# Optimization experiments

Measured on AMD Instinct MI355X. Metric: run time of the kernel, lower is better.

## Reference

```python
import jax, jax.numpy as jnp
import numpy as np

LN_EPS = 1e-5

def _layernorm(x, g, b):
    mu = jnp.mean(x, axis=-1, keepdims=True)
    var = jnp.var(x, axis=-1, keepdims=True)
    return (x - mu) * jax.lax.rsqrt(var + LN_EPS) * g + b

def setup_inputs() -> dict:
    key = jax.random.key(0)
    ks = jax.random.split(key, 8)
    B, N, n, m, a = 4096, 50000, 1024, 16384, 256
    return {
        "x": jax.random.normal(ks[0], (B, n), dtype=jnp.float32),
        "X_data": jax.random.normal(ks[1], (N, n), dtype=jnp.float32),
        "memory_indices": jax.random.randint(ks[2], (m,), 0, N, dtype=jnp.int64)
            if jax.config.jax_enable_x64 else jax.random.randint(ks[2], (m,), 0, N, dtype=jnp.int32),
        "W_q": jax.random.normal(ks[3], (a, n), dtype=jnp.float32) / np.sqrt(n),
        "W_k": jax.random.normal(ks[4], (a, n), dtype=jnp.float32) / np.sqrt(n),
        "W_v": jax.random.normal(ks[5], (n, n), dtype=jnp.float32) / np.sqrt(n),
        "g_q": jnp.ones((a,), jnp.float32), "b_q": jnp.zeros((a,), jnp.float32),
        "g_k": jnp.ones((a,), jnp.float32), "b_k": jnp.zeros((a,), jnp.float32),
        "g_v": jnp.ones((n,), jnp.float32), "b_v": jnp.zeros((n,), jnp.float32),
    }

def reference(x, X_data, memory_indices, W_q, W_k, W_v, g_q, b_q, g_k, b_k, g_v, b_v):
    # Gather memory bank rows: [m, n]
    X_cross = X_data[memory_indices]
    n = x.shape[-1]
    # preprocess(): scalar normalizer so mean row norm ~= sqrt(n) (SAE convention)
    C = jnp.mean(jnp.linalg.norm(X_cross, axis=-1)) / jnp.sqrt(jnp.asarray(n, x.dtype))
    X_cross = X_cross / C
    xs = x / C
    # QKV projections (Linear, no bias) + per-stream LayerNorm
    q = _layernorm(xs @ W_q.T, g_q, b_q)        # [B, a]
    k = _layernorm(X_cross @ W_k.T, g_k, b_k)   # [m, a]
    v = _layernorm(X_cross @ W_v.T, g_v, b_v)   # [m, n]
    # scaled dot-product attention over the memory bank
    scale = 1.0 / np.sqrt(q.shape[-1])
    attn = jax.nn.softmax(jnp.einsum('ba,ma->bm', q, k) * scale, axis=-1)  # [B, m]
    x_hat = attn @ v                             # [B, n]
    return (xs, x_hat, attn, v)
```

## Files before the change

### kernel.cpp

```cpp
#include <hip/hip_runtime.h>
#include <math.h>

typedef _Float16 hlf4 __attribute__((ext_vector_type(4)));
typedef _Float16 hlf8 __attribute__((ext_vector_type(8)));
typedef float f32x4 __attribute__((ext_vector_type(4)));

static __device__ __forceinline__ void gl_lds16(const void* g, void* l) {
    __builtin_amdgcn_global_load_lds(
        (const __attribute__((address_space(1))) unsigned int*)g,
        (__attribute__((address_space(3))) unsigned int*)l, 16, 0, 0);
}

static __device__ __forceinline__ float blk_sum(float v) {
    __shared__ float sm[256];
    int tid = threadIdx.x;
    sm[tid] = v; __syncthreads();
#pragma unroll
    for (int s = 128; s > 0; s >>= 1) {
        if (tid < s) sm[tid] += sm[tid + s];
        __syncthreads();
    }
    float r = sm[0]; __syncthreads();
    return r;
}

static __device__ __forceinline__ float blk_max(float v) {
    __shared__ float sm[256];
    int tid = threadIdx.x;
    sm[tid] = v; __syncthreads();
#pragma unroll
    for (int s = 128; s > 0; s >>= 1) {
        if (tid < s) sm[tid] = fmaxf(sm[tid], sm[tid + s]);
        __syncthreads();
    }
    float r = sm[0]; __syncthreads();
    return r;
}

__global__ __launch_bounds__(256) void k_row_norms(
    const float* __restrict__ X, const int* __restrict__ idx,
    float* __restrict__ norms, int n) {
    long long r = idx[blockIdx.x];
    const float* xr = X + r * (long long)n;
    float s = 0.f;
    for (int k = threadIdx.x * 4; k < n; k += 256 * 4) {
        float4 v = *(const float4*)(xr + k);
        s = fmaf(v.x, v.x, s); s = fmaf(v.y, v.y, s);
        s = fmaf(v.z, v.z, s); s = fmaf(v.w, v.w, s);
    }
    float tot = blk_sum(s);
    if (threadIdx.x == 0) norms[blockIdx.x] = sqrtf(tot);
}

__global__ __launch_bounds__(256) void k_cinv(
    const float* __restrict__ norms, int m, int n, float* __restrict__ cinv) {
    float s = 0.f;
    for (int i = threadIdx.x; i < m; i += 256) s += norms[i];
    float tot = blk_sum(s);
    if (threadIdx.x == 0) cinv[0] = (float)m * sqrtf((float)n) / tot;
}

__global__ __launch_bounds__(256) void k_scale2(
    const float* __restrict__ x, const float* __restrict__ cinv,
    float* __restrict__ y, _Float16* __restrict__ yh, long long total4) {
    float c = cinv[0];
    long long i = blockIdx.x * 256ll + threadIdx.x;
    long long stride = (long long)gridDim.x * 256ll;
    for (; i < total4; i += stride) {
        float4 v = ((const float4*)x)[i];
        float4 w = {v.x * c, v.y * c, v.z * c, v.w * c};
        ((float4*)y)[i] = w;
        hlf4 o = {(_Float16)v.x, (_Float16)v.y, (_Float16)v.z, (_Float16)v.w};
        ((hlf4*)yh)[i] = o;
    }
}

__global__ __launch_bounds__(256) void k_gather_cvt(
    const float* __restrict__ X, const int* __restrict__ idx,
    _Float16* __restrict__ out, int n) {
    long long r = idx[blockIdx.x];
    const float* src = X + r * (long long)n;
    _Float16* dst = out + (long long)blockIdx.x * n;
    for (int k = threadIdx.x * 4; k < n; k += 256 * 4) {
        float4 v = *(const float4*)(src + k);
        hlf4 o = {(_Float16)v.x, (_Float16)v.y, (_Float16)v.z, (_Float16)v.w};
        *(hlf4*)(dst + k) = o;
    }
}

__global__ __launch_bounds__(256) void k_cvt(
    const float* __restrict__ in, _Float16* __restrict__ out, long long n4,
    float sc) {
    long long i = blockIdx.x * 256ll + threadIdx.x;
    long long stride = (long long)gridDim.x * 256ll;
    for (; i < n4; i += stride) {
        float4 v = ((const float4*)in)[i];
        hlf4 o = {(_Float16)(v.x * sc), (_Float16)(v.y * sc),
                  (_Float16)(v.z * sc), (_Float16)(v.w * sc)};
        ((hlf4*)out)[i] = o;
    }
}

__global__ __launch_bounds__(256) void k_tcvt(
    const float* __restrict__ in, _Float16* __restrict__ out, int R, int Cc) {
    __shared__ _Float16 t[32][34];
    int tx = threadIdx.x & 31, ty = threadIdx.x >> 5;
    int c0 = blockIdx.x * 32, r0 = blockIdx.y * 32;
#pragma unroll
    for (int i = 0; i < 32; i += 8)
        t[ty + i][tx] = (_Float16)in[(long long)(r0 + ty + i) * Cc + c0 + tx];
    __syncthreads();
#pragma unroll
    for (int i = 0; i < 32; i += 8)
        out[(long long)(c0 + ty + i) * R + r0 + tx] = t[tx][ty + i];
}

template <int MODE>
__global__ __launch_bounds__(256) void k_gemm4(
    const _Float16* __restrict__ A, int lda,
    const _Float16* __restrict__ B, int ldb,
    void* __restrict__ Cc, long long ldc, int K,
    float* __restrict__ part, long long zstride) {
    __shared__ _Float16 Ah[2][4096];
    __shared__ _Float16 Bh[2][4096];
    const int tid = threadIdx.x;
    const long long m0 = (long long)blockIdx.x * 128;
    const long long n0 = (long long)blockIdx.y * 128;
    const int KC = K / gridDim.z;
    const int kbase = blockIdx.z * KC;
    const int lane = tid & 63, wv = tid >> 6;
    const int wm = (wv >> 1) * 64, wn = (wv & 1) * 64;
    const int fr = lane & 15, fq = lane >> 4;

    const int s0 = tid, s1 = tid + 256;
    const int r0s = s0 >> 2, r1s = s1 >> 2;
    const int g0 = (((s0 & 3) ^ (r0s & 3)) << 3);
    const int g1 = (((s1 & 3) ^ (r1s & 3)) << 3);
    const _Float16* A0 = A + (m0 + r0s) * (long long)lda + kbase + g0;
    const _Float16* A1 = A + (m0 + r1s) * (long long)lda + kbase + g1;
    const _Float16* B0 = B + (n0 + r0s) * (long long)ldb + kbase + g0;
    const _Float16* B1 = B + (n0 + r1s) * (long long)ldb + kbase + g1;

    f32x4 acc[4][4] = {};

    const int NT = KC / 32;
    {
        gl_lds16(A0, &Ah[0][wv * 512]);
        gl_lds16(A1, &Ah[0][2048 + wv * 512]);
        gl_lds16(B0, &Bh[0][wv * 512]);
        gl_lds16(B1, &Bh[0][2048 + wv * 512]);
    }
    __syncthreads();

    for (int kt = 0; kt < NT; ++kt) {
        const int cur = kt & 1;
        if (kt + 1 < NT) {
            const int nx = cur ^ 1;
            const long long ko = (long long)(kt + 1) * 32;
            gl_lds16(A0 + ko, &Ah[nx][wv * 512]);
            gl_lds16(A1 + ko, &Ah[nx][2048 + wv * 512]);
            gl_lds16(B0 + ko, &Bh[nx][wv * 512]);
            gl_lds16(B1 + ko, &Bh[nx][2048 + wv * 512]);
        }
        hlf8 af[4], bf[4];
#pragma unroll
        for (int i = 0; i < 4; ++i) {
            const int r = wm + i * 16 + fr;
            af[i] = *(const hlf8*)&Ah[cur][r * 32 + ((fq ^ (r & 3)) << 3)];
        }
#pragma unroll
        for (int j = 0; j < 4; ++j) {
            const int r = wn + j * 16 + fr;
            bf[j] = *(const hlf8*)&Bh[cur][r * 32 + ((fq ^ (r & 3)) << 3)];
        }
#pragma unroll
        for (int i = 0; i < 4; ++i)
#pragma unroll
            for (int j = 0; j < 4; ++j)
                acc[i][j] = __builtin_amdgcn_mfma_f32_16x16x32_f16(af[i], bf[j], acc[i][j], 0, 0, 0);
        __syncthreads();
    }

    if constexpr (MODE == 1) {
        _Float16* op = (_Float16*)Cc;
#pragma unroll
        for (int i = 0; i < 4; ++i)
#pragma unroll
            for (int j = 0; j < 4; ++j) {
                _Float16* cp = op + (m0 + wm + i * 16 + fq * 4) * ldc + (n0 + wn + j * 16 + fr);
#pragma unroll
                for (int r = 0; r < 4; ++r)
                    cp[(long long)r * ldc] = (_Float16)__expf(acc[i][j][r] - 5.0f);
            }
    } else {
        float* outp = (gridDim.z == 1) ? (float*)Cc : (part + (long long)blockIdx.z * zstride);
#pragma unroll
        for (int i = 0; i < 4; ++i)
#pragma unroll
            for (int j = 0; j < 4; ++j) {
                float* cp = outp + (m0 + wm + i * 16 + fq * 4) * ldc + (n0 + wn + j * 16 + fr);
#pragma unroll
                for (int r = 0; r < 4; ++r) cp[(long long)r * ldc] = acc[i][j][r];
            }
    }
}

__global__ __launch_bounds__(256) void k_redux(
    const float* __restrict__ part, float* __restrict__ out,
    long long n4, long long zs4, int Z,
    const float* __restrict__ invs, int rowdiv4) {
    long long i = blockIdx.x * 256ll + threadIdx.x;
    long long stride = (long long)gridDim.x * 256ll;
    for (; i < n4; i += stride) {
        float4 s = ((const float4*)part)[i];
        for (int z = 1; z < Z; ++z) {
            float4 t = ((const float4*)part)[i + z * zs4];
            s.x += t.x; s.y += t.y; s.z += t.z; s.w += t.w;
        }
        if (invs) {
            float iv = invs[i / rowdiv4];
            s.x *= iv; s.y *= iv; s.z *= iv; s.w *= iv;
        }
        ((float4*)out)[i] = s;
    }
}

template <int CNT>
__global__ __launch_bounds__(256) void k_layernorm(
    float* __restrict__ Y, const float* __restrict__ g,
    const float* __restrict__ b, int W) {
    float* yr = Y + (long long)blockIdx.x * W;
    float v[CNT];
    float s = 0.f;
#pragma unroll
    for (int i = 0; i < CNT; ++i) {
        v[i] = yr[threadIdx.x + (i << 8)];
        s += v[i];
    }
    float mu = blk_sum(s) / (float)W;
    float sq = 0.f;
#pragma unroll
    for (int i = 0; i < CNT; ++i) {
        float d = v[i] - mu;
        sq = fmaf(d, d, sq);
    }
    float var = blk_sum(sq) / (float)W;
    float rs = rsqrtf(var + 1e-5f);
#pragma unroll
    for (int i = 0; i < CNT; ++i) {
        int col = threadIdx.x + (i << 8);
        yr[col] = (v[i] - mu) * rs * g[col] + b[col];
    }
}

__global__ __launch_bounds__(256) void k_softmax_e(
    const _Float16* __restrict__ E, float* __restrict__ attnf,
    float* __restrict__ invs) {
    const _Float16* er = E + (long long)blockIdx.x * 16384;
    float* ar = attnf + (long long)blockIdx.x * 16384;
    float4 r[16];
    float sum = 0.f;
#pragma unroll
    for (int i = 0; i < 16; ++i) {
        hlf4 h = ((const hlf4*)er)[threadIdx.x + (i << 8)];
        float4 t = {(float)h[0], (float)h[1], (float)h[2], (float)h[3]};
        r[i] = t;
        sum += t.x + t.y + t.z + t.w;
    }
    sum = blk_sum(sum);
    float inv = 1.0f / sum;
    if (threadIdx.x == 0) invs[blockIdx.x] = inv;
#pragma unroll
    for (int i = 0; i < 16; ++i) {
        float4 t = r[i];
        t.x *= inv; t.y *= inv; t.z *= inv; t.w *= inv;
        ((float4*)ar)[threadIdx.x + (i << 8)] = t;
    }
}

__global__ __launch_bounds__(256) void k_softmax(
    float* __restrict__ S, _Float16* __restrict__ Sh, float scale) {
    float* sr = S + (long long)blockIdx.x * 16384;
    _Float16* shr = Sh ? Sh + (long long)blockIdx.x * 16384 : nullptr;
    float4 r[16];
    float mx = -1e30f;
#pragma unroll
    for (int i = 0; i < 16; ++i) {
        float4 t = ((const float4*)sr)[threadIdx.x + (i << 8)];
        t.x *= scale; t.y *= scale; t.z *= scale; t.w *= scale;
        r[i] = t;
        mx = fmaxf(mx, fmaxf(fmaxf(t.x, t.y), fmaxf(t.z, t.w)));
    }
    mx = blk_max(mx);
    float sum = 0.f;
#pragma unroll
    for (int i = 0; i < 16; ++i) {
        float4 t = r[i];
        t.x = __expf(t.x - mx); t.y = __expf(t.y - mx);
        t.z = __expf(t.z - mx); t.w = __expf(t.w - mx);
        r[i] = t;
        sum += t.x + t.y + t.z + t.w;
    }
    sum = blk_sum(sum);
    float inv = 1.0f / sum;
#pragma unroll
    for (int i = 0; i < 16; ++i) {
        float4 t = r[i];
        t.x *= inv; t.y *= inv; t.z *= inv; t.w *= inv;
        ((float4*)sr)[threadIdx.x + (i << 8)] = t;
        if (shr) {
            hlf4 o = {(_Float16)t.x, (_Float16)t.y, (_Float16)t.z, (_Float16)t.w};
            ((hlf4*)shr)[threadIdx.x + (i << 8)] = o;
        }
    }
}

extern "C" void kernel_launch(void* const* d_in, const int* in_sizes, int n_in,
                              void* d_out, int out_size, void* d_ws, size_t ws_size,
                              hipStream_t stream) {
    const float* x      = (const float*)d_in[0];
    const float* X_data = (const float*)d_in[1];
    const int*   midx   = (const int*)d_in[2];
    const float* W_q    = (const float*)d_in[3];
    const float* W_k    = (const float*)d_in[4];
    const float* W_v    = (const float*)d_in[5];
    const float* g_q    = (const float*)d_in[6];
    const float* b_q    = (const float*)d_in[7];
    const float* g_k    = (const float*)d_in[8];
    const float* b_k    = (const float*)d_in[9];
    const float* g_v    = (const float*)d_in[10];
    const float* b_v    = (const float*)d_in[11];

    const int n  = in_sizes[10];
    const int a  = in_sizes[6];
    const int m  = in_sizes[2];
    const int Bn = in_sizes[0] / n;

    float* out  = (float*)d_out;
    float* xs   = out;
    float* xhat = xs + (long long)Bn * n;
    float* attn = xhat + (long long)Bn * n;
    float* vout = attn + (long long)Bn * m;

    char* wp = (char*)d_ws;
    auto carve = [&](size_t bytes) -> char* {
        char* r = wp; wp += (bytes + 255) & ~(size_t)255; return r;
    };
    float*     norms = (float*)carve((size_t)m * 4);
    float*     cinv  = (float*)carve(16);
    float*     invs  = (float*)carve((size_t)Bn * 4);
    char*      alias0 = wp;
    float*     qmat  = (float*)carve((size_t)Bn * a * 4);
    float*     kmat  = (float*)carve((size_t)m * a * 4);
    _Float16*  xs_h  = (_Float16*)carve((size_t)Bn * n * 2);
    _Float16*  Xc_h  = (_Float16*)carve((size_t)m * n * 2);
    _Float16*  Wq_h  = (_Float16*)carve((size_t)a * n * 2);
    _Float16*  Wk_h  = (_Float16*)carve((size_t)a * n * 2);
    _Float16*  Wv_h  = (_Float16*)carve((size_t)n * n * 2);
    _Float16*  q_h   = (_Float16*)carve((size_t)Bn * a * 2);
    _Float16*  k_h   = (_Float16*)carve((size_t)m * a * 2);
    float*     splitk = (float*)alias0;
    const int  SK = 4;
    _Float16*  vT_h  = (_Float16*)carve((size_t)n * m * 2);
    size_t used = (size_t)(wp - (char*)d_ws);
    _Float16* attn_h = nullptr;
    if (ws_size >= used + (size_t)Bn * m * 2 + 256)
        attn_h = (_Float16*)carve((size_t)Bn * m * 2);

    hipLaunchKernelGGL(k_gather_cvt, dim3(m), dim3(256), 0, stream,
                       X_data, midx, Xc_h, n);
    hipLaunchKernelGGL(k_row_norms, dim3(m), dim3(256), 0, stream, X_data, midx, norms, n);
    hipLaunchKernelGGL(k_cinv, dim3(1), dim3(256), 0, stream, norms, m, n, cinv);

    hipLaunchKernelGGL(k_scale2, dim3(2048), dim3(256), 0, stream,
                       x, cinv, xs, xs_h, (long long)Bn * n / 4);

    hipLaunchKernelGGL(k_cvt, dim3(256), dim3(256), 0, stream, W_q, Wq_h, (long long)a * n / 4, 1.f);
    hipLaunchKernelGGL(k_cvt, dim3(256), dim3(256), 0, stream, W_k, Wk_h, (long long)a * n / 4, 1.f);
    hipLaunchKernelGGL(k_cvt, dim3(1024), dim3(256), 0, stream, W_v, Wv_h, (long long)n * n / 4, 1.f);

    hipLaunchKernelGGL((k_gemm4<0>), dim3(Bn / 128, a / 128), dim3(256), 0, stream,
                       xs_h, n, Wq_h, n, qmat, a, n, (float*)nullptr, 0ll);
    hipLaunchKernelGGL((k_gemm4<0>), dim3(m / 128, a / 128), dim3(256), 0, stream,
                       Xc_h, n, Wk_h, n, kmat, a, n, (float*)nullptr, 0ll);
    hipLaunchKernelGGL((k_gemm4<0>), dim3(m / 128, n / 128), dim3(256), 0, stream,
                       Xc_h, n, Wv_h, n, vout, n, n, (float*)nullptr, 0ll);

    float sc = 1.0f / sqrtf((float)a);
    hipLaunchKernelGGL(k_layernorm<1>, dim3(Bn), dim3(256), 0, stream, qmat, g_q, b_q, a);
    hipLaunchKernelGGL(k_layernorm<1>, dim3(m),  dim3(256), 0, stream, kmat, g_k, b_k, a);
    hipLaunchKernelGGL(k_layernorm<4>, dim3(m),  dim3(256), 0, stream, vout, g_v, b_v, n);
    hipLaunchKernelGGL(k_cvt, dim3(1024), dim3(256), 0, stream, qmat, q_h, (long long)Bn * a / 4, sc);
    hipLaunchKernelGGL(k_cvt, dim3(4096), dim3(256), 0, stream, kmat, k_h, (long long)m * a / 4, 1.f);
    hipLaunchKernelGGL(k_tcvt, dim3(n / 32, m / 32), dim3(256), 0, stream, vout, vT_h, m, n);

    long long zstride = (long long)Bn * n;
    if (attn_h) {
        hipLaunchKernelGGL((k_gemm4<1>), dim3(Bn / 128, m / 128), dim3(256), 0, stream,
                           q_h, a, k_h, a, attn_h, m, a, (float*)nullptr, 0ll);
        hipLaunchKernelGGL(k_softmax_e, dim3(Bn), dim3(256), 0, stream,
                           attn_h, attn, invs);
        hipLaunchKernelGGL((k_gemm4<0>), dim3(Bn / 128, n / 128, SK), dim3(256), 0, stream,
                           attn_h, m, vT_h, m, xhat, n, m, splitk, zstride);
        hipLaunchKernelGGL(k_redux, dim3(2048), dim3(256), 0, stream,
                           splitk, xhat, (long long)Bn * n / 4, zstride / 4, SK,
                           invs, n / 4);
    } else {
        hipLaunchKernelGGL((k_gemm4<0>), dim3(Bn / 128, m / 128), dim3(256), 0, stream,
                           q_h, a, k_h, a, attn, m, a, (float*)nullptr, 0ll);
        hipLaunchKernelGGL(k_softmax, dim3(Bn), dim3(256), 0, stream, attn, (_Float16*)nullptr, 1.0f);
        _Float16* chunk_h = (_Float16*)splitk;
        for (int cb = 0; cb < 4; ++cb) {
            const float* src = attn + (long long)cb * 1024 * m;
            hipLaunchKernelGGL(k_cvt, dim3(4096), dim3(256), 0, stream,
                               src, chunk_h, (long long)1024 * m / 4, 1.f);
            hipLaunchKernelGGL((k_gemm4<0>), dim3(1024 / 128, n / 128), dim3(256), 0, stream,
                               chunk_h, m, vT_h, m, xhat + (long long)cb * 1024 * n, n, m,
                               (float*)nullptr, 0ll);
        }
    }
}
```

Before: 570.6 us.

## Fuse row norms into gather, fuse LN with fp16 cvt, swizzle GEMM blocks

Row-norm computation moves into the gather/convert kernel so the gathered rows are read once instead of twice. The q/k layernorm is fused with the fp16 conversion and scale, which drops two conversion passes. The GEMM remaps block indices into an XCD-aware swizzled order, aimed at better L2 locality across the chiplets. The fallback path now uses the exp-in-epilogue GEMM plus softmax_e per chunk with a final normalisation, which brings several unrelated changes together.

```diff
diff --git a/kernel.cpp b/kernel.cpp
--- a/kernel.cpp
+++ b/kernel.cpp
@@ -35,21 +35,6 @@
     }
     float r = sm[0]; __syncthreads();
     return r;
-}
-
-__global__ __launch_bounds__(256) void k_row_norms(
-    const float* __restrict__ X, const int* __restrict__ idx,
-    float* __restrict__ norms, int n) {
-    long long r = idx[blockIdx.x];
-    const float* xr = X + r * (long long)n;
-    float s = 0.f;
-    for (int k = threadIdx.x * 4; k < n; k += 256 * 4) {
-        float4 v = *(const float4*)(xr + k);
-        s = fmaf(v.x, v.x, s); s = fmaf(v.y, v.y, s);
-        s = fmaf(v.z, v.z, s); s = fmaf(v.w, v.w, s);
-    }
-    float tot = blk_sum(s);
-    if (threadIdx.x == 0) norms[blockIdx.x] = sqrtf(tot);
 }
 
 __global__ __launch_bounds__(256) void k_cinv(
@@ -77,15 +62,20 @@
 
 __global__ __launch_bounds__(256) void k_gather_cvt(
     const float* __restrict__ X, const int* __restrict__ idx,
-    _Float16* __restrict__ out, int n) {
+    _Float16* __restrict__ out, float* __restrict__ norms, int n) {
     long long r = idx[blockIdx.x];
     const float* src = X + r * (long long)n;
     _Float16* dst = out + (long long)blockIdx.x * n;
+    float s = 0.f;
     for (int k = threadIdx.x * 4; k < n; k += 256 * 4) {
         float4 v = *(const float4*)(src + k);
         hlf4 o = {(_Float16)v.x, (_Float16)v.y, (_Float16)v.z, (_Float16)v.w};
         *(hlf4*)(dst + k) = o;
-    }
+        s = fmaf(v.x, v.x, s); s = fmaf(v.y, v.y, s);
+        s = fmaf(v.z, v.z, s); s = fmaf(v.w, v.w, s);
+    }
+    float tot = blk_sum(s);
+    if (threadIdx.x == 0) norms[blockIdx.x] = sqrtf(tot);
 }
 
 __global__ __launch_bounds__(256) void k_cvt(
@@ -124,10 +114,19 @@
     __shared__ _Float16 Ah[2][4096];
     __shared__ _Float16 Bh[2][4096];
     const int tid = threadIdx.x;
-    const long long m0 = (long long)blockIdx.x * 128;
-    const long long n0 = (long long)blockIdx.y * 128;
+
+    const int gx = gridDim.x, gy = gridDim.y;
+    int lin = blockIdx.x + gx * (blockIdx.y + gy * blockIdx.z);
+    const int cpx = (gx * gy * (int)gridDim.z) >> 3;
+    lin = (lin & 7) * cpx + (lin >> 3);
+    const int by = lin % gy;
+    const int rest = lin / gy;
+    const int bx = rest % gx, bz = rest / gx;
+
+    const long long m0 = (long long)bx * 128;
+    const long long n0 = (long long)by * 128;
     const int KC = K / gridDim.z;
-    const int kbase = blockIdx.z * KC;
+    const int kbase = bz * KC;
     const int lane = tid & 63, wv = tid >> 6;
     const int wm = (wv >> 1) * 64, wn = (wv & 1) * 64;
     const int fr = lane & 15, fq = lane >> 4;
@@ -193,7 +192,7 @@
                     cp[(long long)r * ldc] = (_Float16)__expf(acc[i][j][r] - 5.0f);
             }
     } else {
-        float* outp = (gridDim.z == 1) ? (float*)Cc : (part + (long long)blockIdx.z * zstride);
+        float* outp = (gridDim.z == 1) ? (float*)Cc : (part + (long long)bz * zstride);
 #pragma unroll
         for (int i = 0; i < 4; ++i)
 #pragma unroll
@@ -253,6 +252,19 @@
     }
 }
 
+__global__ __launch_bounds__(256) void k_layernorm_h(
+    const float* __restrict__ Y, const float* __restrict__ g,
+    const float* __restrict__ b, _Float16* __restrict__ outh, int W, float sc) {
+    const float* yr = Y + (long long)blockIdx.x * W;
+    _Float16* orow = outh + (long long)blockIdx.x * W;
+    float v = yr[threadIdx.x];
+    float mu = blk_sum(v) / (float)W;
+    float d = v - mu;
+    float var = blk_sum(d * d) / (float)W;
+    float rs = rsqrtf(var + 1e-5f);
+    orow[threadIdx.x] = (_Float16)((d * rs * g[threadIdx.x] + b[threadIdx.x]) * sc);
+}
+
 __global__ __launch_bounds__(256) void k_softmax_e(
     const _Float16* __restrict__ E, float* __restrict__ attnf,
     float* __restrict__ invs) {
@@ -275,43 +287,6 @@
         float4 t = r[i];
         t.x *= inv; t.y *= inv; t.z *= inv; t.w *= inv;
         ((float4*)ar)[threadIdx.x + (i << 8)] = t;
-    }
-}
-
-__global__ __launch_bounds__(256) void k_softmax(
-    float* __restrict__ S, _Float16* __restrict__ Sh, float scale) {
-    float* sr = S + (long long)blockIdx.x * 16384;
-    _Float16* shr = Sh ? Sh + (long long)blockIdx.x * 16384 : nullptr;
-    float4 r[16];
-    float mx = -1e30f;
-#pragma unroll
-    for (int i = 0; i < 16; ++i) {
-        float4 t = ((const float4*)sr)[threadIdx.x + (i << 8)];
-        t.x *= scale; t.y *= scale; t.z *= scale; t.w *= scale;
-        r[i] = t;
-        mx = fmaxf(mx, fmaxf(fmaxf(t.x, t.y), fmaxf(t.z, t.w)));
-    }
-    mx = blk_max(mx);
-    float sum = 0.f;
-#pragma unroll
-    for (int i = 0; i < 16; ++i) {
-        float4 t = r[i];
-        t.x = __expf(t.x - mx); t.y = __expf(t.y - mx);
-        t.z = __expf(t.z - mx); t.w = __expf(t.w - mx);
-        r[i] = t;
-        sum += t.x + t.y + t.z + t.w;
-    }
-    sum = blk_sum(sum);
-    float inv = 1.0f / sum;
-#pragma unroll
-    for (int i = 0; i < 16; ++i) {
-        float4 t = r[i];
-        t.x *= inv; t.y *= inv; t.z *= inv; t.w *= inv;
-        ((float4*)sr)[threadIdx.x + (i << 8)] = t;
-        if (shr) {
-            hlf4 o = {(_Float16)t.x, (_Float16)t.y, (_Float16)t.z, (_Float16)t.w};
-            ((hlf4*)shr)[threadIdx.x + (i << 8)] = o;
-        }
     }
 }
 
@@ -368,8 +343,7 @@
         attn_h = (_Float16*)carve((size_t)Bn * m * 2);
 
     hipLaunchKernelGGL(k_gather_cvt, dim3(m), dim3(256), 0, stream,
-                       X_data, midx, Xc_h, n);
-    hipLaunchKernelGGL(k_row_norms, dim3(m), dim3(256), 0, stream, X_data, midx, norms, n);
+                       X_data, midx, Xc_h, norms, n);
     hipLaunchKernelGGL(k_cinv, dim3(1), dim3(256), 0, stream, norms, m, n, cinv);
 
     hipLaunchKernelGGL(k_scale2, dim3(2048), dim3(256), 0, stream,
@@ -387,11 +361,11 @@
                        Xc_h, n, Wv_h, n, vout, n, n, (float*)nullptr, 0ll);
 
     float sc = 1.0f / sqrtf((float)a);
-    hipLaunchKernelGGL(k_layernorm<1>, dim3(Bn), dim3(256), 0, stream, qmat, g_q, b_q, a);
-    hipLaunchKernelGGL(k_layernorm<1>, dim3(m),  dim3(256), 0, stream, kmat, g_k, b_k, a);
-    hipLaunchKernelGGL(k_layernorm<4>, dim3(m),  dim3(256), 0, stream, vout, g_v, b_v, n);
-    hipLaunchKernelGGL(k_cvt, dim3(1024), dim3(256), 0, stream, qmat, q_h, (long long)Bn * a / 4, sc);
-    hipLaunchKernelGGL(k_cvt, dim3(4096), dim3(256), 0, stream, kmat, k_h, (long long)m * a / 4, 1.f);
+    hipLaunchKernelGGL(k_layernorm_h, dim3(Bn), dim3(256), 0, stream,
+                       qmat, g_q, b_q, q_h, a, sc);
+    hipLaunchKernelGGL(k_layernorm_h, dim3(m), dim3(256), 0, stream,
+                       kmat, g_k, b_k, k_h, a, 1.f);
+    hipLaunchKernelGGL(k_layernorm<4>, dim3(m), dim3(256), 0, stream, vout, g_v, b_v, n);
     hipLaunchKernelGGL(k_tcvt, dim3(n / 32, m / 32), dim3(256), 0, stream, vout, vT_h, m, n);
 
     long long zstride = (long long)Bn * n;
@@ -406,17 +380,19 @@
                            splitk, xhat, (long long)Bn * n / 4, zstride / 4, SK,
                            invs, n / 4);
     } else {
-        hipLaunchKernelGGL((k_gemm4<0>), dim3(Bn / 128, m / 128), dim3(256), 0, stream,
-                           q_h, a, k_h, a, attn, m, a, (float*)nullptr, 0ll);
-        hipLaunchKernelGGL(k_softmax, dim3(Bn), dim3(256), 0, stream, attn, (_Float16*)nullptr, 1.0f);
         _Float16* chunk_h = (_Float16*)splitk;
         for (int cb = 0; cb < 4; ++cb) {
-            const float* src = attn + (long long)cb * 1024 * m;
-            hipLaunchKernelGGL(k_cvt, dim3(4096), dim3(256), 0, stream,
-                               src, chunk_h, (long long)1024 * m / 4, 1.f);
+            hipLaunchKernelGGL((k_gemm4<1>), dim3(1024 / 128, m / 128), dim3(256), 0, stream,
+                               q_h + (long long)cb * 1024 * a, a, k_h, a,
+                               chunk_h, m, a, (float*)nullptr, 0ll);
+            hipLaunchKernelGGL(k_softmax_e, dim3(1024), dim3(256), 0, stream,
+                               chunk_h, attn + (long long)cb * 1024 * m,
+                               invs + (long long)cb * 1024);
             hipLaunchKernelGGL((k_gemm4<0>), dim3(1024 / 128, n / 128), dim3(256), 0, stream,
                                chunk_h, m, vT_h, m, xhat + (long long)cb * 1024 * n, n, m,
                                (float*)nullptr, 0ll);
         }
-    }
-}
+        hipLaunchKernelGGL(k_redux, dim3(2048), dim3(256), 0, stream,
+                           xhat, xhat, (long long)Bn * n / 4, 0ll, 1, invs, n / 4);
+    }
+}
```

New measurement: 552.4 us. 3.2% less time.
